# Performance work log

Measured on AMD Instinct MI355X. Metric: run time of the kernel, lower is better.

Reference implementation:

```python
import jax, jax.numpy as jnp
import numpy as np

T, B, DIN, H, AA, L = 1024, 32, 256, 256, 21, 2


def setup_inputs() -> dict:
    key = jax.random.key(0)
    ks = jax.random.split(key, 8)
    scale = 0.05

    def rn(i, shape):
        return jax.random.normal(ks[i], shape, dtype=jnp.float32) * scale

    return {
        "x": jax.random.normal(ks[0], (B, T, DIN), dtype=jnp.float32),
        "hidden": jnp.zeros((2 * L, B, H), jnp.float32),  # accepted but unused, as in torch forward
        # layer 0: input DIN -> per-direction 4 chunks of H; layer 1: input 2H
        "w_l0": rn(1, (DIN, 2, 4, H)),
        "wc_l0": rn(2, (2, 2, H)),            # [dir, (v_f, v_r), H]
        "b_l0": jnp.zeros((2, 2, H), jnp.float32),  # [dir, (b_f, b_r), H]
        "w_l1": rn(3, (2 * H, 2, 4, H)),
        "wc_l1": rn(4, (2, 2, H)),
        "b_l1": jnp.zeros((2, 2, H), jnp.float32),
        "fc1_w": rn(5, (H, 2 * H)),
        "fc1_b": jnp.zeros((H,), jnp.float32),
        "lp_w": rn(6, (AA, H)),
        "lp_b": jnp.zeros((AA,), jnp.float32),
    }


def _sru_scan(u, vf, vr, bf, br):
    # u: (T, B, 4, H) with chunks [candidate, forget, reset, highway]
    def step(c, ut):
        f = jax.nn.sigmoid(ut[:, 1] + vf * c + bf)
        c2 = f * c + (1.0 - f) * ut[:, 0]
        r = jax.nn.sigmoid(ut[:, 2] + vr * c + br)
        h = r * c2 + (1.0 - r) * ut[:, 3]
        return c2, h

    c0 = jnp.zeros((u.shape[1], u.shape[-1]), u.dtype)
    _, hs = jax.lax.scan(step, c0, u)
    return hs  # (T, B, H)


def _sru_layer(x, w, wc, b):
    # x: (T, B, Din); w: (Din, 2, 4, H)
    U = jnp.einsum('tbd,dnkh->tbnkh', x, w)
    hf = _sru_scan(U[:, :, 0], wc[0, 0], wc[0, 1], b[0, 0], b[0, 1])
    hb = _sru_scan(U[::-1, :, 1], wc[1, 0], wc[1, 1], b[1, 0], b[1, 1])[::-1]
    return jnp.concatenate([hf, hb], axis=-1)  # (T, B, 2H)


def reference(x, hidden, w_l0, wc_l0, b_l0, w_l1, wc_l1, b_l1, fc1_w, fc1_b, lp_w, lp_b):
    h = jnp.transpose(x, (1, 0, 2))  # (T, B, DIN)
    h = _sru_layer(h, w_l0, wc_l0, b_l0)
    h = _sru_layer(h, w_l1, wc_l1, b_l1)
    h = jnp.transpose(h, (1, 0, 2))  # (B, T, 2H)
    h = h @ fc1_w.T + fc1_b
    logits = h @ lp_w.T + lp_b
    return jax.nn.log_softmax(logits, axis=-1)  # (B, T, AA)
```

## Files before the change

### kernel.cpp

```cpp
#include <hip/hip_runtime.h>
#include <hip/hip_bf16.h>

#define T_DIM 1024
#define B_DIM 32
#define DIN_DIM 256
#define H_DIM 256
#define AA_DIM 21
#define M_ROWS (B_DIM * T_DIM)

typedef __attribute__((ext_vector_type(8))) short bf16x8;
typedef __attribute__((ext_vector_type(4))) float f32x4;

typedef __attribute__((address_space(3))) void lds_void;
typedef const __attribute__((address_space(1))) void glb_void;

#define LOG2E_F 1.44269504088896340736f

__device__ __forceinline__ void gload_lds16(const void* g, void* l) {
    __builtin_amdgcn_global_load_lds((glb_void*)g, (lds_void*)l, 16, 0, 0);
}

__device__ __forceinline__ float b2f(unsigned short v) {
    unsigned u = ((unsigned)v) << 16;
    float f;
    __builtin_memcpy(&f, &u, 4);
    return f;
}

__device__ __forceinline__ unsigned short f2bu(float f) {
    __hip_bfloat16 h = __float2bfloat16(f);
    unsigned short u;
    __builtin_memcpy(&u, &h, 2);
    return u;
}

#define CVT_V0 2097152
#define CVT_N1 524288
#define CVT_N2 1048576
#define CVT_V3 32768
#define CVT_N4 8192
#define CVT_N5 4096
#define CVT_TOT (CVT_V0 + CVT_N1 + CVT_N2 + CVT_V3 + CVT_N4 + CVT_N5)
__global__ __launch_bounds__(256) void cvt_all(
    const float* __restrict__ x,  const float* __restrict__ w0,
    const float* __restrict__ w1, const float* __restrict__ fcw,
    const float* __restrict__ lpw,
    const float* __restrict__ b0, const float* __restrict__ b1,
    __hip_bfloat16* __restrict__ xb,  __hip_bfloat16* __restrict__ w0t,
    __hip_bfloat16* __restrict__ w1t, __hip_bfloat16* __restrict__ fcwb,
    __hip_bfloat16* __restrict__ lpwb,
    float* __restrict__ sc0, float* __restrict__ bs0,
    float* __restrict__ sc1, float* __restrict__ bs1)
{
    int i = blockIdx.x * 256 + threadIdx.x;
    if (i < CVT_V0) {
        float4 v = ((const float4*)x)[i];
        ushort4 o = { f2bu(v.x), f2bu(v.y), f2bu(v.z), f2bu(v.w) };
        ((ushort4*)xb)[i] = o;
        return;
    }
    i -= CVT_V0;
    if (i < CVT_N1) {
        int kk = i >> 11, rem = i & 2047;
        int dir = rem >> 10, k = (rem >> 8) & 3, h = rem & 255;
        w0t[(long)(dir * 1024 + h * 4 + k) * 256 + kk] = __float2bfloat16(w0[i]);
        return;
    }
    i -= CVT_N1;
    if (i < CVT_N2) {
        int kk = i >> 11, rem = i & 2047;
        int dir = rem >> 10, k = (rem >> 8) & 3, h = rem & 255;
        w1t[(long)(dir * 1024 + h * 4 + k) * 512 + kk] = __float2bfloat16(w1[i]);
        return;
    }
    i -= CVT_N2;
    if (i < CVT_V3) {
        float4 v = ((const float4*)fcw)[i];
        ushort4 o = { f2bu(v.x), f2bu(v.y), f2bu(v.z), f2bu(v.w) };
        ((ushort4*)fcwb)[i] = o;
        return;
    }
    i -= CVT_V3;
    if (i < CVT_N4) {
        int n = i >> 8, k = i & 255;
        lpwb[i] = __float2bfloat16(n < AA_DIM ? lpw[n * 256 + k] : 0.0f);
        return;
    }
    i -= CVT_N4;
    if (i < CVT_N5) {
        int layer = i >> 11, n = i & 2047;
        int k = n & 3, h = (n >> 2) & 255, dir = n >> 10;
        const float* bb = layer ? b1 : b0;
        float sc = 1.0f, bs = 0.0f;
        if (k == 1) { sc = -LOG2E_F; bs = -LOG2E_F * bb[(dir * 2 + 0) * 256 + h]; }
        if (k == 2) { sc = -LOG2E_F; bs = -LOG2E_F * bb[(dir * 2 + 1) * 256 + h]; }
        if (layer) { sc1[n] = sc; bs1[n] = bs; }
        else       { sc0[n] = sc; bs0[n] = bs; }
    }
}

__global__ __launch_bounds__(256) void gemm_bf16(
    const __hip_bfloat16* __restrict__ A,
    const __hip_bfloat16* __restrict__ Bt,
    const float* __restrict__ bias,
    const float* __restrict__ scale,
    __hip_bfloat16* __restrict__ C,
    int M, int N, int K, int nbShift)
{
    __shared__ __align__(16) char smb[32768];

    const int tid  = threadIdx.x;
    const int lane = tid & 63;
    const int wave = tid >> 6;
    const int wm = wave & 1;
    const int wn = wave >> 1;

    const int L   = blockIdx.x;
    const int s   = L >> 3;
    const int nb  = s & ((1 << nbShift) - 1);
    const int mb  = ((s >> nbShift) << 3) + (L & 7);
    const long n0 = (long)nb * 128;
    const long m0 = (long)mb * 128;

    f32x4 acc[4][4] = {};

    const int ldrow = lane >> 2;
    const int ldq   = lane & 3;
    const int gq    = ldq ^ ((ldrow >> 1) & 3);
    const int gkoff = gq * 8;

    const int fr = lane & 15;
    const int kq = lane >> 4;
    const int sw = (kq ^ ((fr >> 1) & 3)) * 16;

    for (int kb = 0; kb < K; kb += 64) {
        __syncthreads();
#pragma unroll
        for (int i = 0; i < 4; ++i) {
            const int cid = wave * 4 + i;
            const int rc  = cid >> 1;
            const int kh  = cid & 1;
            const long row = rc * 16 + ldrow;
            const int koff = kb + kh * 32 + gkoff;
            gload_lds16(A  + (m0 + row) * (long)K + koff,
                        smb + rc * 2048 + kh * 1024);
            gload_lds16(Bt + (n0 + row) * (long)K + koff,
                        smb + 16384 + rc * 2048 + kh * 1024);
        }
        __syncthreads();

#pragma unroll
        for (int ss = 0; ss < 2; ++ss) {
            bf16x8 af[4], bfv[4];
#pragma unroll
            for (int i = 0; i < 4; ++i) {
                af[i]  = *(const bf16x8*)(smb + (wm * 4 + i) * 2048 + ss * 1024 + fr * 64 + sw);
                bfv[i] = *(const bf16x8*)(smb + 16384 + (wn * 4 + i) * 2048 + ss * 1024 + fr * 64 + sw);
            }
#pragma unroll
            for (int i = 0; i < 4; ++i)
#pragma unroll
                for (int j = 0; j < 4; ++j)
                    acc[i][j] = __builtin_amdgcn_mfma_f32_16x16x32_bf16(
                        af[i], bfv[j], acc[i][j], 0, 0, 0);
        }
    }

    const int col_l = lane & 15;
    const int row_l = (lane >> 4) * 4;
    __hip_bfloat16* smC = (__hip_bfloat16*)smb;
#pragma unroll
    for (int p = 0; p < 2; ++p) {
        __syncthreads();
        if (wm == p) {
#pragma unroll
            for (int j = 0; j < 4; ++j) {
                const long gc = n0 + wn * 64 + j * 16 + col_l;
                const float bv = bias ? bias[gc] : 0.0f;
                const float av = scale ? scale[gc] : 1.0f;
#pragma unroll
                for (int i = 0; i < 4; ++i)
#pragma unroll
                    for (int r = 0; r < 4; ++r)
                        smC[(i * 16 + row_l + r) * 132 + wn * 64 + j * 16 + col_l] =
                            __float2bfloat16(__builtin_fmaf(acc[i][j][r], av, bv));
            }
        }
        __syncthreads();
        const int cb = (tid & 7) * 16;
#pragma unroll
        for (int s2 = 0; s2 < 2; ++s2) {
            const int rr = s2 * 32 + (tid >> 3);
            const long gr = m0 + p * 64 + rr;
            bf16x8 v0 = *(const bf16x8*)(smC + rr * 132 + cb);
            bf16x8 v1 = *(const bf16x8*)(smC + rr * 132 + cb + 8);
            *(bf16x8*)(C + gr * (long)N + n0 + cb)     = v0;
            *(bf16x8*)(C + gr * (long)N + n0 + cb + 8) = v1;
        }
    }
}

#define SCAN_PF 32
template<int DIR>
__device__ __forceinline__ void scan_body(
    const __hip_bfloat16* __restrict__ U,
    const float* __restrict__ wc,
    __hip_bfloat16* __restrict__ hout, int id)
{
    const int rem = id & 8191;
    const int b   = rem >> 8;
    const int h   = rem & 255;

    const float nvf = -LOG2E_F * wc[(DIR * 2 + 0) * H_DIM + h];
    const float nvr = -LOG2E_F * wc[(DIR * 2 + 1) * H_DIM + h];

    const long row0 = (long)b * T_DIM + (DIR ? (T_DIM - 1) : 0);
    constexpr long PSTEP = DIR ? -512L : 512L;
    constexpr long HSTEP = DIR ? -512L : 512L;

    const uint2* __restrict__ p = (const uint2*)(U + row0 * 2048 + DIR * 1024 + (h << 2));
    __hip_bfloat16* __restrict__ hcur = hout + row0 * 512 + DIR * 256 + h;

    uint2 buf[SCAN_PF];
#pragma unroll
    for (int j = 0; j < SCAN_PF; ++j) buf[j] = p[(long)j * PSTEP];
    const uint2* __restrict__ pl = p + (long)SCAN_PF * PSTEP;

    float c = 0.0f;
    for (int s0 = 0; s0 < T_DIM - SCAN_PF; s0 += SCAN_PF) {
#pragma unroll
        for (int j = 0; j < SCAN_PF; ++j) {
            const uint2 u = buf[j];
            buf[j] = pl[(long)j * PSTEP];
            float u0, u1s, u2s, u3;
            {
                unsigned a0 = u.x << 16, a1 = u.x & 0xffff0000u;
                unsigned a2 = u.y << 16, a3 = u.y & 0xffff0000u;
                __builtin_memcpy(&u0, &a0, 4); __builtin_memcpy(&u1s, &a1, 4);
                __builtin_memcpy(&u2s, &a2, 4); __builtin_memcpy(&u3, &a3, 4);
            }
            const float ef = __builtin_amdgcn_exp2f(__builtin_fmaf(nvf, c, u1s));
            const float er = __builtin_amdgcn_exp2f(__builtin_fmaf(nvr, c, u2s));
            const float f  = __builtin_amdgcn_rcpf(1.0f + ef);
            const float r  = __builtin_amdgcn_rcpf(1.0f + er);
            const float c2 = __builtin_fmaf(f, c - u0, u0);
            const float hv = __builtin_fmaf(r, c2 - u3, u3);
            c = c2;
            hcur[(long)j * HSTEP] = __float2bfloat16(hv);
        }
        pl   += (long)SCAN_PF * PSTEP;
        hcur += (long)SCAN_PF * HSTEP;
    }
#pragma unroll
    for (int j = 0; j < SCAN_PF; ++j) {
        const uint2 u = buf[j];
        float u0, u1s, u2s, u3;
        {
            unsigned a0 = u.x << 16, a1 = u.x & 0xffff0000u;
            unsigned a2 = u.y << 16, a3 = u.y & 0xffff0000u;
            __builtin_memcpy(&u0, &a0, 4); __builtin_memcpy(&u1s, &a1, 4);
            __builtin_memcpy(&u2s, &a2, 4); __builtin_memcpy(&u3, &a3, 4);
        }
        const float ef = __builtin_amdgcn_exp2f(__builtin_fmaf(nvf, c, u1s));
        const float er = __builtin_amdgcn_exp2f(__builtin_fmaf(nvr, c, u2s));
        const float f  = __builtin_amdgcn_rcpf(1.0f + ef);
        const float r  = __builtin_amdgcn_rcpf(1.0f + er);
        const float c2 = __builtin_fmaf(f, c - u0, u0);
        const float hv = __builtin_fmaf(r, c2 - u3, u3);
        c = c2;
        hcur[(long)j * HSTEP] = __float2bfloat16(hv);
    }
}

__global__ __launch_bounds__(64) void sru_scan(
    const __hip_bfloat16* __restrict__ U,
    const float* __restrict__ wc,
    __hip_bfloat16* __restrict__ hout)
{
    const int id = blockIdx.x * 64 + threadIdx.x;
    if (id < 8192) scan_body<0>(U, wc, hout, id);
    else           scan_body<1>(U, wc, hout, id);
}

__global__ __launch_bounds__(256) void logits_mfma(
    const __hip_bfloat16* __restrict__ fc,
    const __hip_bfloat16* __restrict__ lpwb,
    const float* __restrict__ lpb,
    float* __restrict__ out)
{
    __shared__ __align__(16) char smb[25088];
    const int tid  = threadIdx.x;
    const int lane = tid & 63;
    const int wave = tid >> 6;
    const long m0  = (long)blockIdx.x * 128;

    for (int idx = tid; idx < 32 * 32; idx += 256) {
        const int rw = idx >> 5, sl = idx & 31;
        *(bf16x8*)(smb + rw * 528 + sl * 16) =
            *(const bf16x8*)(lpwb + rw * 256 + sl * 8);
    }

    const int ldrow = lane >> 2;
    const int ldq   = lane & 3;
    const int gq    = ldq ^ ((ldrow >> 1) & 3);
    const int gkoff = gq * 8;

    const int fr = lane & 15;
    const int kq = lane >> 4;
    const int sw = (kq ^ ((fr >> 1) & 3)) * 16;

    f32x4 acc[2][2] = {};
    for (int kc = 0; kc < 8; ++kc) {
        __syncthreads();
#pragma unroll
        for (int i = 0; i < 2; ++i) {
            const int rc = wave * 2 + i;
            gload_lds16(fc + (m0 + rc * 16 + ldrow) * 256 + kc * 32 + gkoff,
                        smb + 16896 + rc * 1024);
        }
        __syncthreads();
        bf16x8 af[2], bfv[2];
#pragma unroll
        for (int i = 0; i < 2; ++i)
            af[i] = *(const bf16x8*)(smb + 16896 + (wave * 2 + i) * 1024 + fr * 64 + sw);
#pragma unroll
        for (int j = 0; j < 2; ++j)
            bfv[j] = *(const bf16x8*)(smb + (j * 16 + fr) * 528 + kc * 64 + kq * 16);
#pragma unroll
        for (int i = 0; i < 2; ++i)
#pragma unroll
            for (int j = 0; j < 2; ++j)
                acc[i][j] = __builtin_amdgcn_mfma_f32_16x16x32_bf16(
                    af[i], bfv[j], acc[i][j], 0, 0, 0);
    }

    __syncthreads();
    float* smC = (float*)smb;
    const int col_l = lane & 15;
    const int row_l = (lane >> 4) * 4;
#pragma unroll
    for (int j = 0; j < 2; ++j) {
        const int gc = j * 16 + col_l;
        const float bv = (gc < AA_DIM) ? lpb[gc] : 0.0f;
#pragma unroll
        for (int i = 0; i < 2; ++i)
#pragma unroll
            for (int r = 0; r < 4; ++r)
                smC[(wave * 32 + i * 16 + row_l + r) * 36 + gc] = acc[i][j][r] + bv;
    }
    __syncthreads();
    if (tid < 128) {
        const float* rowp = smC + tid * 36;
        float m = rowp[0];
#pragma unroll
        for (int a = 1; a < AA_DIM; ++a) m = fmaxf(m, rowp[a]);
        float s = 0.0f;
#pragma unroll
        for (int a = 0; a < AA_DIM; ++a) s += __expf(rowp[a] - m);
        const float lse = __logf(s) + m;
        float* op = out + (m0 + tid) * AA_DIM;
#pragma unroll
        for (int a = 0; a < AA_DIM; ++a) op[a] = rowp[a] - lse;
    }
}

extern "C" void kernel_launch(void* const* d_in, const int* in_sizes, int n_in,
                              void* d_out, int out_size, void* d_ws, size_t ws_size,
                              hipStream_t stream)
{
    const float* x     = (const float*)d_in[0];
    const float* w_l0  = (const float*)d_in[2];
    const float* wc_l0 = (const float*)d_in[3];
    const float* b_l0  = (const float*)d_in[4];
    const float* w_l1  = (const float*)d_in[5];
    const float* wc_l1 = (const float*)d_in[6];
    const float* b_l1  = (const float*)d_in[7];
    const float* fc1_w = (const float*)d_in[8];
    const float* fc1_b = (const float*)d_in[9];
    const float* lp_w  = (const float*)d_in[10];
    const float* lp_b  = (const float*)d_in[11];
    float* out = (float*)d_out;

    char* ws = (char*)d_ws;
    __hip_bfloat16* U      = (__hip_bfloat16*)(ws);
    __hip_bfloat16* h0b    = (__hip_bfloat16*)(ws + 134217728);
    __hip_bfloat16* h1b    = (__hip_bfloat16*)(ws + 167772160);
    __hip_bfloat16* xb     = (__hip_bfloat16*)(ws + 201326592);
    __hip_bfloat16* fcob   = xb;
    __hip_bfloat16* w0t    = (__hip_bfloat16*)(ws + 218103808);
    __hip_bfloat16* w1t    = (__hip_bfloat16*)(ws + 219152384);
    __hip_bfloat16* fc1wb  = (__hip_bfloat16*)(ws + 221249536);
    __hip_bfloat16* lpwb   = (__hip_bfloat16*)(ws + 221511680);
    float* sc0 = (float*)(ws + 221528064);
    float* bs0 = (float*)(ws + 221536256);
    float* sc1 = (float*)(ws + 221544448);
    float* bs1 = (float*)(ws + 221552640);

    cvt_all<<<(CVT_TOT + 255) / 256, 256, 0, stream>>>(
        x, w_l0, w_l1, fc1_w, lp_w, b_l0, b_l1,
        xb, w0t, w1t, fc1wb, lpwb, sc0, bs0, sc1, bs1);

    gemm_bf16<<<4096, 256, 0, stream>>>(
        xb, w0t, bs0, sc0, U, M_ROWS, 2048, DIN_DIM, 4);
    sru_scan<<<256, 64, 0, stream>>>(U, wc_l0, h0b);
    gemm_bf16<<<4096, 256, 0, stream>>>(
        h0b, w1t, bs1, sc1, U, M_ROWS, 2048, 512, 4);
    sru_scan<<<256, 64, 0, stream>>>(U, wc_l1, h1b);
    gemm_bf16<<<512, 256, 0, stream>>>(
        h1b, fc1wb, fc1_b, nullptr, fcob, M_ROWS, 256, 512, 1);
    logits_mfma<<<M_ROWS / 128, 256, 0, stream>>>(fcob, lpwb, lp_b, out);
}
```

Measured before the change: 419.7 us.

## Relayout U per scan slice and stage scan inputs via LDS producer waves

```diff
diff --git a/kernel.cpp b/kernel.cpp
--- a/kernel.cpp
+++ b/kernel.cpp
@@ -99,6 +99,7 @@
     }
 }
 
+template<int U2OUT>
 __global__ __launch_bounds__(256) void gemm_bf16(
     const __hip_bfloat16* __restrict__ A,
     const __hip_bfloat16* __restrict__ Bt,
@@ -194,92 +195,95 @@
             const long gr = m0 + p * 64 + rr;
             bf16x8 v0 = *(const bf16x8*)(smC + rr * 132 + cb);
             bf16x8 v1 = *(const bf16x8*)(smC + rr * 132 + cb + 8);
-            *(bf16x8*)(C + gr * (long)N + n0 + cb)     = v0;
-            *(bf16x8*)(C + gr * (long)N + n0 + cb + 8) = v1;
-        }
-    }
-}
-
-#define SCAN_PF 32
-template<int DIR>
-__device__ __forceinline__ void scan_body(
-    const __hip_bfloat16* __restrict__ U,
-    const float* __restrict__ wc,
-    __hip_bfloat16* __restrict__ hout, int id)
-{
-    const int rem = id & 8191;
-    const int b   = rem >> 8;
-    const int h   = rem & 255;
-
-    const float nvf = -LOG2E_F * wc[(DIR * 2 + 0) * H_DIM + h];
-    const float nvr = -LOG2E_F * wc[(DIR * 2 + 1) * H_DIM + h];
-
-    const long row0 = (long)b * T_DIM + (DIR ? (T_DIM - 1) : 0);
-    constexpr long PSTEP = DIR ? -512L : 512L;
-    constexpr long HSTEP = DIR ? -512L : 512L;
-
-    const uint2* __restrict__ p = (const uint2*)(U + row0 * 2048 + DIR * 1024 + (h << 2));
-    __hip_bfloat16* __restrict__ hcur = hout + row0 * 512 + DIR * 256 + h;
-
-    uint2 buf[SCAN_PF];
-#pragma unroll
-    for (int j = 0; j < SCAN_PF; ++j) buf[j] = p[(long)j * PSTEP];
-    const uint2* __restrict__ pl = p + (long)SCAN_PF * PSTEP;
-
-    float c = 0.0f;
-    for (int s0 = 0; s0 < T_DIM - SCAN_PF; s0 += SCAN_PF) {
-#pragma unroll
-        for (int j = 0; j < SCAN_PF; ++j) {
-            const uint2 u = buf[j];
-            buf[j] = pl[(long)j * PSTEP];
-            float u0, u1s, u2s, u3;
-            {
-                unsigned a0 = u.x << 16, a1 = u.x & 0xffff0000u;
-                unsigned a2 = u.y << 16, a3 = u.y & 0xffff0000u;
-                __builtin_memcpy(&u0, &a0, 4); __builtin_memcpy(&u1s, &a1, 4);
-                __builtin_memcpy(&u2s, &a2, 4); __builtin_memcpy(&u3, &a3, 4);
+            if (U2OUT) {
+                const int bI  = (int)(gr >> 10);
+                const int t   = (int)(gr & 1023);
+                const long gc0 = n0 + cb;
+                const int dir = (int)(gc0 >> 10);
+                const int hg  = ((int)gc0 >> 8) & 3;
+                const int beta = bI * 8 + dir * 4 + hg;
+                const long base = ((long)beta * 1024 + t) * 256 + (gc0 & 255);
+                *(bf16x8*)(C + base)     = v0;
+                *(bf16x8*)(C + base + 8) = v1;
+            } else {
+                *(bf16x8*)(C + gr * (long)N + n0 + cb)     = v0;
+                *(bf16x8*)(C + gr * (long)N + n0 + cb + 8) = v1;
             }
-            const float ef = __builtin_amdgcn_exp2f(__builtin_fmaf(nvf, c, u1s));
-            const float er = __builtin_amdgcn_exp2f(__builtin_fmaf(nvr, c, u2s));
-            const float f  = __builtin_amdgcn_rcpf(1.0f + ef);
-            const float r  = __builtin_amdgcn_rcpf(1.0f + er);
-            const float c2 = __builtin_fmaf(f, c - u0, u0);
-            const float hv = __builtin_fmaf(r, c2 - u3, u3);
-            c = c2;
-            hcur[(long)j * HSTEP] = __float2bfloat16(hv);
-        }
-        pl   += (long)SCAN_PF * PSTEP;
-        hcur += (long)SCAN_PF * HSTEP;
-    }
-#pragma unroll
-    for (int j = 0; j < SCAN_PF; ++j) {
-        const uint2 u = buf[j];
-        float u0, u1s, u2s, u3;
-        {
-            unsigned a0 = u.x << 16, a1 = u.x & 0xffff0000u;
-            unsigned a2 = u.y << 16, a3 = u.y & 0xffff0000u;
-            __builtin_memcpy(&u0, &a0, 4); __builtin_memcpy(&u1s, &a1, 4);
-            __builtin_memcpy(&u2s, &a2, 4); __builtin_memcpy(&u3, &a3, 4);
-        }
-        const float ef = __builtin_amdgcn_exp2f(__builtin_fmaf(nvf, c, u1s));
-        const float er = __builtin_amdgcn_exp2f(__builtin_fmaf(nvr, c, u2s));
-        const float f  = __builtin_amdgcn_rcpf(1.0f + ef);
-        const float r  = __builtin_amdgcn_rcpf(1.0f + er);
-        const float c2 = __builtin_fmaf(f, c - u0, u0);
-        const float hv = __builtin_fmaf(r, c2 - u3, u3);
-        c = c2;
-        hcur[(long)j * HSTEP] = __float2bfloat16(hv);
-    }
-}
-
-__global__ __launch_bounds__(64) void sru_scan(
-    const __hip_bfloat16* __restrict__ U,
+        }
+    }
+}
+
+#define SCAN_S 64
+#define SCAN_NB (T_DIM / SCAN_S)
+__global__ __launch_bounds__(256) void sru_scan(
+    const __hip_bfloat16* __restrict__ U2,
     const float* __restrict__ wc,
     __hip_bfloat16* __restrict__ hout)
 {
-    const int id = blockIdx.x * 64 + threadIdx.x;
-    if (id < 8192) scan_body<0>(U, wc, hout, id);
-    else           scan_body<1>(U, wc, hout, id);
+    __shared__ __align__(16) char lds[2 * SCAN_S * 512];
+    const int tid  = threadIdx.x;
+    const int wave = tid >> 6;
+    const int lane = tid & 63;
+    const int beta = blockIdx.x;
+    const int b    = beta >> 3;
+    const int dir  = (beta >> 2) & 1;
+    const int hg   = beta & 3;
+    const int h    = hg * 64 + lane;
+
+    const char* gslice = (const char*)U2 + (size_t)beta * (1024 * 512);
+
+    const float nvf = -LOG2E_F * wc[(dir * 2 + 0) * H_DIM + h];
+    const float nvr = -LOG2E_F * wc[(dir * 2 + 1) * H_DIM + h];
+    __hip_bfloat16* hp = hout + ((long)(b * 1024 + (dir ? 1023 : 0))) * 512 + dir * 256 + h;
+    const long hstep = dir ? -512L : 512L;
+    float c = 0.0f;
+
+    if (wave > 0) {
+        for (int s2 = wave - 1; s2 < SCAN_S; s2 += 3) {
+            const int t = dir ? (1023 - s2) : s2;
+            uint2 v = *(const uint2*)(gslice + (size_t)t * 512 + (lane << 3));
+            *(uint2*)(lds + s2 * 512 + (lane << 3)) = v;
+        }
+    }
+    __syncthreads();
+
+    for (int bat = 0; bat < SCAN_NB; ++bat) {
+        if (wave > 0) {
+            if (bat + 1 < SCAN_NB) {
+                char* half = lds + ((bat + 1) & 1) * (SCAN_S * 512);
+                const int tb = (bat + 1) * SCAN_S;
+                for (int s2 = wave - 1; s2 < SCAN_S; s2 += 3) {
+                    const int tl = tb + s2;
+                    const int t  = dir ? (1023 - tl) : tl;
+                    uint2 v = *(const uint2*)(gslice + (size_t)t * 512 + (lane << 3));
+                    *(uint2*)(half + s2 * 512 + (lane << 3)) = v;
+                }
+            }
+        } else {
+            const char* half = lds + (bat & 1) * (SCAN_S * 512);
+            __hip_bfloat16* hq = hp + (long)(bat * SCAN_S) * hstep;
+#pragma unroll 8
+            for (int s2 = 0; s2 < SCAN_S; ++s2) {
+                const uint2 u = *(const uint2*)(half + s2 * 512 + (lane << 3));
+                float u0, u1s, u2s, u3;
+                {
+                    unsigned a0 = u.x << 16, a1 = u.x & 0xffff0000u;
+                    unsigned a2 = u.y << 16, a3 = u.y & 0xffff0000u;
+                    __builtin_memcpy(&u0, &a0, 4); __builtin_memcpy(&u1s, &a1, 4);
+                    __builtin_memcpy(&u2s, &a2, 4); __builtin_memcpy(&u3, &a3, 4);
+                }
+                const float ef = __builtin_amdgcn_exp2f(__builtin_fmaf(nvf, c, u1s));
+                const float er = __builtin_amdgcn_exp2f(__builtin_fmaf(nvr, c, u2s));
+                const float f  = __builtin_amdgcn_rcpf(1.0f + ef);
+                const float r  = __builtin_amdgcn_rcpf(1.0f + er);
+                const float c2 = __builtin_fmaf(f, c - u0, u0);
+                const float hv = __builtin_fmaf(r, c2 - u3, u3);
+                c = c2;
+                hq[(long)s2 * hstep] = __float2bfloat16(hv);
+            }
+        }
+        __syncthreads();
+    }
 }
 
 __global__ __launch_bounds__(256) void logits_mfma(
@@ -400,13 +404,13 @@
         x, w_l0, w_l1, fc1_w, lp_w, b_l0, b_l1,
         xb, w0t, w1t, fc1wb, lpwb, sc0, bs0, sc1, bs1);
 
-    gemm_bf16<<<4096, 256, 0, stream>>>(
+    gemm_bf16<1><<<4096, 256, 0, stream>>>(
         xb, w0t, bs0, sc0, U, M_ROWS, 2048, DIN_DIM, 4);
-    sru_scan<<<256, 64, 0, stream>>>(U, wc_l0, h0b);
-    gemm_bf16<<<4096, 256, 0, stream>>>(
+    sru_scan<<<256, 256, 0, stream>>>(U, wc_l0, h0b);
+    gemm_bf16<1><<<4096, 256, 0, stream>>>(
         h0b, w1t, bs1, sc1, U, M_ROWS, 2048, 512, 4);
-    sru_scan<<<256, 64, 0, stream>>>(U, wc_l1, h1b);
-    gemm_bf16<<<512, 256, 0, stream>>>(
+    sru_scan<<<256, 256, 0, stream>>>(U, wc_l1, h1b);
+    gemm_bf16<0><<<512, 256, 0, stream>>>(
         h1b, fc1wb, fc1_b, nullptr, fcob, M_ROWS, 256, 512, 1);
     logits_mfma<<<M_ROWS / 128, 256, 0, stream>>>(fcob, lpwb, lp_b, out);
 }
```

New measurement: 483.7 us. 15.3% more time.
